# Kernel optimization log

Hardware: AMD Instinct MI355X
Metric: run time of the kernel (lower is better)

The kernel has to match this reference:

```python
import jax, jax.numpy as jnp
import numpy as np

NUM_GRAPHS = 1024


def setup_inputs() -> dict:
    key = jax.random.key(0)
    k1, k2, k3, k4 = jax.random.split(key, 4)
    N, D, H = 500000, 256, 256
    x = jax.random.normal(k1, (N, D), dtype=jnp.float32)
    batch = jnp.sort(jax.random.randint(k2, (N,), 0, NUM_GRAPHS, dtype=jnp.int64))
    # Linear init scale ~ 1/sqrt(fan_in)
    W1 = jax.random.normal(k3, (D, H), dtype=jnp.float32) / np.sqrt(D)
    b1 = jnp.zeros((H,), dtype=jnp.float32)
    W2 = jax.random.normal(k4, (H, 1), dtype=jnp.float32) / np.sqrt(H)
    b2 = jnp.zeros((1,), dtype=jnp.float32)
    return {"x": x, "batch": batch, "W1": W1, "b1": b1, "W2": W2, "b2": b2}


def reference(x, batch, W1, b1, W2, b2):
    # Two-layer attention MLP -> scores [N, 1] (dropout = identity at eval)
    scores = jnp.tanh(x @ W1 + b1) @ W2 + b2
    # Softmax over dim 0 (global over all nodes, as in the source)
    attn = jax.nn.softmax(scores, axis=0)  # [N, 1]
    # Weighted scatter-add pooling per graph id
    pooled = jax.ops.segment_sum(x * attn, batch, num_segments=NUM_GRAPHS)
    return pooled  # [NUM_GRAPHS, D]
```

## Files before the change

### kernel.cpp

```cpp
#include <hip/hip_runtime.h>
#include <stdint.h>

#define NBLOCKS 256
#define WPB 16
#define SLOTS (NBLOCKS * WPB)
#define SMEM_BYTES (131072 + 2048)

typedef __attribute__((ext_vector_type(8))) short bfrag_t;
typedef __attribute__((ext_vector_type(4))) float f32x4;

static __device__ __forceinline__ unsigned short f2bf(float f) {
  unsigned int u = __float_as_uint(f);
  u += 0x7fffu + ((u >> 16) & 1u);
  return (unsigned short)(u >> 16);
}

static __device__ __forceinline__ float tanh_fast(float s) {
  float e = __builtin_exp2f(s * 2.8853900817779268f);
  float r = __builtin_amdgcn_rcpf(1.f + e);
  return __builtin_fmaf(-2.f, r, 1.f);
}

static __device__ __forceinline__ float readlane_f(float v, int l) {
  return __uint_as_float(__builtin_amdgcn_readlane(__float_as_uint(v), l));
}

static __device__ __forceinline__ bfrag_t pack8(f32x4 a, f32x4 b) {
  union { bfrag_t v; unsigned int u[4]; } r;
  asm("v_cvt_pk_bf16_f32 %0, %1, %2" : "=v"(r.u[0]) : "v"(a[0]), "v"(a[1]));
  asm("v_cvt_pk_bf16_f32 %0, %1, %2" : "=v"(r.u[1]) : "v"(a[2]), "v"(a[3]));
  asm("v_cvt_pk_bf16_f32 %0, %1, %2" : "=v"(r.u[2]) : "v"(b[0]), "v"(b[1]));
  asm("v_cvt_pk_bf16_f32 %0, %1, %2" : "=v"(r.u[3]) : "v"(b[2]), "v"(b[3]));
  return r.v;
}

#define KEEPA(A) asm volatile("" : "+v"(A[0]), "+v"(A[1]), "+v"(A[2]), "+v"(A[3]), \
                                    "+v"(A[4]), "+v"(A[5]), "+v"(A[6]), "+v"(A[7]))

#define GLD16(gp, lp) __builtin_amdgcn_global_load_lds( \
    (const __attribute__((address_space(1))) void*)(gp), \
    (__attribute__((address_space(3))) void*)(lp), 16, 0, 0)

__global__ void prep_w1_kernel(const float* __restrict__ W1, unsigned short* __restrict__ W1f) {
  const int bx = blockIdx.x;
  const int l = threadIdx.x;
  const int cc = bx >> 3, kk = bx & 7;
  const int h = cc * 16 + (l & 15);
  const int kbase = kk * 32 + ((l >> 4) << 3);
  bfrag_t pk;
#pragma unroll
  for (int j = 0; j < 8; ++j) pk[j] = (short)f2bf(W1[(size_t)(kbase + j) * 256 + h]);
  *(bfrag_t*)(W1f + (size_t)(bx * 64 + l) * 8) = pk;
}

__launch_bounds__(1024, 4)
__global__ void attnpool_kernel(const float* __restrict__ x,
                                const int* __restrict__ batch,
                                const unsigned short* __restrict__ W1f,
                                const float* __restrict__ b1,
                                const float* __restrict__ W2,
                                const float* __restrict__ b2,
                                float* __restrict__ out,
                                float* __restrict__ Zp,
                                int N, int ntiles, int tps) {
  extern __shared__ char smem[];
  char*  Bl  = smem;
  float* b1s = (float*)(smem + 131072);
  float* w2s = (float*)(smem + 132096);

  const int t = threadIdx.x;
  const int lane = t & 63;
  const int wv = t >> 6;
  const int l15 = lane & 15;
  const int hi = lane >> 4;

#pragma unroll
  for (int i = 0; i < 8; ++i) {
    const int f = wv * 8 + i;
    const unsigned short* src = W1f + (size_t)f * 512 + lane * 8;
    GLD16(src, Bl + f * 1024);
  }
  if (t < 256) { b1s[t] = b1[t]; w2s[t] = W2[t]; }
  __syncthreads();

  const float b2c = b2[0];
  const int slot = blockIdx.x * WPB + wv;
  const int t0 = slot * tps;
  const int t1 = min(t0 + tps, ntiles);

  float zacc = 0.f;
  f32x4 pacc = {0.f, 0.f, 0.f, 0.f};
  int gcur = -1;
  const char* bwave = Bl + lane * 16;

  for (int tile = t0; tile < t1; ++tile) {
    const int R0 = tile * 32;

    int bid = 0;
    {
      int rg = min(R0 + (lane & 31), N - 1);
      bid = batch[rg];
    }

    bfrag_t A0[8], A1[8];
    {
      const int r0g = min(R0 + l15, N - 1);
      const int r1g = min(R0 + 16 + l15, N - 1);
      const float* p0 = x + (size_t)r0g * 256 + hi * 8;
      const float* p1 = x + (size_t)r1g * 256 + hi * 8;
#pragma unroll
      for (int kk = 0; kk < 8; ++kk) {
        const f32x4 u0 = *(const f32x4*)(p0 + kk * 32);
        const f32x4 u1 = *(const f32x4*)(p0 + kk * 32 + 4);
        const f32x4 v0 = *(const f32x4*)(p1 + kk * 32);
        const f32x4 v1 = *(const f32x4*)(p1 + kk * 32 + 4);
        A0[kk] = pack8(u0, u1);
        A1[kk] = pack8(v0, v1);
      }
    }

    float s0[4] = {0.f, 0.f, 0.f, 0.f};
    float s1[4] = {0.f, 0.f, 0.f, 0.f};
#pragma unroll 2
    for (int cc = 0; cc < 16; ++cc) {
      KEEPA(A0);
      KEEPA(A1);
      const char* bb = bwave + cc * 8192;
      f32x4 acc0 = {0.f, 0.f, 0.f, 0.f}, acc1 = {0.f, 0.f, 0.f, 0.f};
#pragma unroll
      for (int kk = 0; kk < 8; ++kk) {
        const bfrag_t Bk = *(const bfrag_t*)(bb + kk * 1024);
        acc0 = __builtin_amdgcn_mfma_f32_16x16x32_bf16(A0[kk], Bk, acc0, 0, 0, 0);
        acc1 = __builtin_amdgcn_mfma_f32_16x16x32_bf16(A1[kk], Bk, acc1, 0, 0, 0);
      }
      const float b1c = b1s[cc * 16 + l15];
      const float w2c = w2s[cc * 16 + l15];
#pragma unroll
      for (int r = 0; r < 4; ++r) {
        s0[r] += tanh_fast(acc0[r] + b1c) * w2c;
        s1[r] += tanh_fast(acc1[r] + b1c) * w2c;
      }
    }

    float w0[4], w1[4];
#pragma unroll
    for (int r = 0; r < 4; ++r) {
      float v0 = s0[r], v1 = s1[r];
      v0 += __shfl_xor(v0, 1); v0 += __shfl_xor(v0, 2);
      v0 += __shfl_xor(v0, 4); v0 += __shfl_xor(v0, 8);
      v1 += __shfl_xor(v1, 1); v1 += __shfl_xor(v1, 2);
      v1 += __shfl_xor(v1, 4); v1 += __shfl_xor(v1, 8);
      w0[r] = (R0 + hi * 4 + r < N) ? __expf(v0 + b2c) : 0.f;
      w1[r] = (R0 + 16 + hi * 4 + r < N) ? __expf(v1 + b2c) : 0.f;
    }
    {
      float z = w0[0] + w0[1] + w0[2] + w0[3] + w1[0] + w1[1] + w1[2] + w1[3];
      z += __shfl_xor(z, 16);
      z += __shfl_xor(z, 32);
      zacc += z;
    }

    const float* xp = x + (size_t)R0 * 256 + lane * 4;
#pragma unroll
    for (int r = 0; r < 32; ++r) {
      const float wr = (r < 16) ? readlane_f(w0[r & 3], ((r >> 2) & 3) * 16)
                                : readlane_f(w1[r & 3], ((r >> 2) & 3) * 16);
      const int g = __builtin_amdgcn_readlane(bid, r);
      if (g != gcur) {
        if (gcur >= 0) {
          float* po = out + (size_t)gcur * 256 + lane * 4;
          atomicAdd(po + 0, pacc[0]); atomicAdd(po + 1, pacc[1]);
          atomicAdd(po + 2, pacc[2]); atomicAdd(po + 3, pacc[3]);
        }
        pacc[0] = pacc[1] = pacc[2] = pacc[3] = 0.f;
        gcur = g;
      }
      const f32x4 xv = *(const f32x4*)(xp + (size_t)r * 256);
      pacc[0] = __builtin_fmaf(wr, xv[0], pacc[0]);
      pacc[1] = __builtin_fmaf(wr, xv[1], pacc[1]);
      pacc[2] = __builtin_fmaf(wr, xv[2], pacc[2]);
      pacc[3] = __builtin_fmaf(wr, xv[3], pacc[3]);
    }
  }

  if (gcur >= 0) {
    float* po = out + (size_t)gcur * 256 + lane * 4;
    atomicAdd(po + 0, pacc[0]); atomicAdd(po + 1, pacc[1]);
    atomicAdd(po + 2, pacc[2]); atomicAdd(po + 3, pacc[3]);
  }
  if (lane == 0 && zacc != 0.f) atomicAdd(Zp, zacc);
}

__global__ void finalize_kernel(float* __restrict__ out, const float* __restrict__ Zp, int n4) {
  const int i = blockIdx.x * blockDim.x + threadIdx.x;
  if (i < n4) {
    const float zi = 1.f / Zp[0];
    f32x4* p = (f32x4*)out;
    f32x4 v = p[i];
    v[0] *= zi; v[1] *= zi; v[2] *= zi; v[3] *= zi;
    p[i] = v;
  }
}

extern "C" void kernel_launch(void* const* d_in, const int* in_sizes, int n_in,
                              void* d_out, int out_size, void* d_ws, size_t ws_size,
                              hipStream_t stream) {
  const float* x  = (const float*)d_in[0];
  const int* batch = (const int*)d_in[1];
  const float* W1 = (const float*)d_in[2];
  const float* b1 = (const float*)d_in[3];
  const float* W2 = (const float*)d_in[4];
  const float* b2 = (const float*)d_in[5];
  float* out = (float*)d_out;
  const int N = in_sizes[1];

  unsigned short* W1f = (unsigned short*)d_ws;
  float* Zp = (float*)((char*)d_ws + 131072);

  static int attr_done = 0;
  if (!attr_done) {
    hipFuncSetAttribute((const void*)attnpool_kernel,
                        hipFuncAttributeMaxDynamicSharedMemorySize, SMEM_BYTES);
    attr_done = 1;
  }

  const int ntiles = (N + 31) / 32;
  const int tps = (ntiles + SLOTS - 1) / SLOTS;

  hipMemsetAsync(d_out, 0, (size_t)out_size * sizeof(float), stream);
  hipMemsetAsync(Zp, 0, sizeof(float), stream);
  prep_w1_kernel<<<128, 64, 0, stream>>>(W1, W1f);
  attnpool_kernel<<<NBLOCKS, 1024, SMEM_BYTES, stream>>>(x, batch, W1f, b1, W2, b2,
                                                         out, Zp, N, ntiles, tps);
  finalize_kernel<<<(out_size / 4 + 255) / 256, 256, 0, stream>>>(out, Zp, out_size / 4);
}
```

Baseline: 214.1 us.

## Reuse bf16 register fragments of x for pooling instead of reloading x

Pooling now accumulates from the bf16 A fragments already held in registers for the MFMA, removing the second global read of x per tile. Per-row weights are broadcast through a small LDS slot, partial sums are reduced with lane shuffles, and multi-graph tiles are handled with masked per-segment passes. This trades memory traffic for extra ALU and shuffle work, and pooling precision drops from fp32 to bf16-rounded x.

```diff
diff --git a/kernel.cpp b/kernel.cpp
--- a/kernel.cpp
+++ b/kernel.cpp
@@ -4,7 +4,7 @@
 #define NBLOCKS 256
 #define WPB 16
 #define SLOTS (NBLOCKS * WPB)
-#define SMEM_BYTES (131072 + 2048)
+#define SMEM_BYTES (131072 + 1024 + 1024 + 2048)
 
 typedef __attribute__((ext_vector_type(8))) short bfrag_t;
 typedef __attribute__((ext_vector_type(4))) float f32x4;
@@ -19,10 +19,6 @@
   float e = __builtin_exp2f(s * 2.8853900817779268f);
   float r = __builtin_amdgcn_rcpf(1.f + e);
   return __builtin_fmaf(-2.f, r, 1.f);
-}
-
-static __device__ __forceinline__ float readlane_f(float v, int l) {
-  return __uint_as_float(__builtin_amdgcn_readlane(__float_as_uint(v), l));
 }
 
 static __device__ __forceinline__ bfrag_t pack8(f32x4 a, f32x4 b) {
@@ -67,6 +63,7 @@
   char*  Bl  = smem;
   float* b1s = (float*)(smem + 131072);
   float* w2s = (float*)(smem + 132096);
+  float* wsl = (float*)(smem + 133120);
 
   const int t = threadIdx.x;
   const int lane = t & 63;
@@ -89,20 +86,82 @@
   const int t1 = min(t0 + tps, ntiles);
 
   float zacc = 0.f;
-  f32x4 pacc = {0.f, 0.f, 0.f, 0.f};
+  float pacc[16];
+#pragma unroll
+  for (int i = 0; i < 16; ++i) pacc[i] = 0.f;
   int gcur = -1;
   const char* bwave = Bl + lane * 16;
+  float* ws = wsl + (wv << 5);
+
+  bfrag_t A0[8], A1[8];
+
+  auto flush = [&]() {
+#pragma unroll
+    for (int i = 0; i < 16; ++i) {
+      pacc[i] += __shfl_xor(pacc[i], 4);
+      pacc[i] += __shfl_xor(pacc[i], 8);
+    }
+    if (l15 < 4) {
+      float* po = out + (size_t)gcur * 256 + hi * 8 + 2 * l15;
+#pragma unroll
+      for (int i = 0; i < 16; ++i)
+        atomicAdd(po + (i >> 1) * 32 + (i & 1), pacc[i]);
+    }
+#pragma unroll
+    for (int i = 0; i < 16; ++i) pacc[i] = 0.f;
+  };
+
+  auto pool_pass = [&](float m0, float m1) {
+    const bool s0 = (l15 & 1) != 0, s1 = (l15 & 2) != 0;
+#pragma unroll
+    for (int half = 0; half < 2; ++half) {
+      float part[4][4][2];
+#pragma unroll
+      for (int k2 = 0; k2 < 4; ++k2) {
+        const int kk = half * 4 + k2;
+        union { bfrag_t v; unsigned int u[4]; } ua, ub;
+        ua.v = A0[kk]; ub.v = A1[kk];
+#pragma unroll
+        for (int q = 0; q < 4; ++q) {
+          const float alo = __uint_as_float(ua.u[q] << 16);
+          const float ahi = __uint_as_float(ua.u[q] & 0xffff0000u);
+          const float blo = __uint_as_float(ub.u[q] << 16);
+          const float bhi = __uint_as_float(ub.u[q] & 0xffff0000u);
+          part[k2][q][0] = __builtin_fmaf(m0, alo, m1 * blo);
+          part[k2][q][1] = __builtin_fmaf(m0, ahi, m1 * bhi);
+        }
+      }
+#pragma unroll
+      for (int k2 = 0; k2 < 4; ++k2)
+#pragma unroll
+        for (int q = 0; q < 4; ++q)
+#pragma unroll
+          for (int p = 0; p < 2; ++p) {
+            float v = part[k2][q][p];
+            v += __shfl_xor(v, 1);
+            v += __shfl_xor(v, 2);
+            part[k2][q][p] = v;
+          }
+#pragma unroll
+      for (int k2 = 0; k2 < 4; ++k2)
+#pragma unroll
+        for (int p = 0; p < 2; ++p) {
+          const float v01 = s0 ? part[k2][1][p] : part[k2][0][p];
+          const float v23 = s0 ? part[k2][3][p] : part[k2][2][p];
+          pacc[(half * 4 + k2) * 2 + p] += s1 ? v23 : v01;
+        }
+    }
+  };
 
   for (int tile = t0; tile < t1; ++tile) {
     const int R0 = tile * 32;
 
-    int bid = 0;
+    int bid;
     {
-      int rg = min(R0 + (lane & 31), N - 1);
+      const int rg = min(R0 + (lane & 31), N - 1);
       bid = batch[rg];
     }
 
-    bfrag_t A0[8], A1[8];
     {
       const int r0g = min(R0 + l15, N - 1);
       const int r1g = min(R0 + 16 + l15, N - 1);
@@ -119,8 +178,8 @@
       }
     }
 
-    float s0[4] = {0.f, 0.f, 0.f, 0.f};
-    float s1[4] = {0.f, 0.f, 0.f, 0.f};
+    float s0v[4] = {0.f, 0.f, 0.f, 0.f};
+    float s1v[4] = {0.f, 0.f, 0.f, 0.f};
 #pragma unroll 2
     for (int cc = 0; cc < 16; ++cc) {
       KEEPA(A0);
@@ -137,57 +196,57 @@
       const float w2c = w2s[cc * 16 + l15];
 #pragma unroll
       for (int r = 0; r < 4; ++r) {
-        s0[r] += tanh_fast(acc0[r] + b1c) * w2c;
-        s1[r] += tanh_fast(acc1[r] + b1c) * w2c;
-      }
-    }
-
-    float w0[4], w1[4];
+        s0v[r] += tanh_fast(acc0[r] + b1c) * w2c;
+        s1v[r] += tanh_fast(acc1[r] + b1c) * w2c;
+      }
+    }
+
+    f32x4 w0v, w1v;
 #pragma unroll
     for (int r = 0; r < 4; ++r) {
-      float v0 = s0[r], v1 = s1[r];
+      float v0 = s0v[r], v1 = s1v[r];
       v0 += __shfl_xor(v0, 1); v0 += __shfl_xor(v0, 2);
       v0 += __shfl_xor(v0, 4); v0 += __shfl_xor(v0, 8);
       v1 += __shfl_xor(v1, 1); v1 += __shfl_xor(v1, 2);
       v1 += __shfl_xor(v1, 4); v1 += __shfl_xor(v1, 8);
-      w0[r] = (R0 + hi * 4 + r < N) ? __expf(v0 + b2c) : 0.f;
-      w1[r] = (R0 + 16 + hi * 4 + r < N) ? __expf(v1 + b2c) : 0.f;
+      w0v[r] = (R0 + hi * 4 + r < N) ? __expf(v0 + b2c) : 0.f;
+      w1v[r] = (R0 + 16 + hi * 4 + r < N) ? __expf(v1 + b2c) : 0.f;
     }
     {
-      float z = w0[0] + w0[1] + w0[2] + w0[3] + w1[0] + w1[1] + w1[2] + w1[3];
+      float z = w0v[0] + w0v[1] + w0v[2] + w0v[3] + w1v[0] + w1v[1] + w1v[2] + w1v[3];
       z += __shfl_xor(z, 16);
       z += __shfl_xor(z, 32);
       zacc += z;
     }
 
-    const float* xp = x + (size_t)R0 * 256 + lane * 4;
-#pragma unroll
-    for (int r = 0; r < 32; ++r) {
-      const float wr = (r < 16) ? readlane_f(w0[r & 3], ((r >> 2) & 3) * 16)
-                                : readlane_f(w1[r & 3], ((r >> 2) & 3) * 16);
-      const int g = __builtin_amdgcn_readlane(bid, r);
-      if (g != gcur) {
-        if (gcur >= 0) {
-          float* po = out + (size_t)gcur * 256 + lane * 4;
-          atomicAdd(po + 0, pacc[0]); atomicAdd(po + 1, pacc[1]);
-          atomicAdd(po + 2, pacc[2]); atomicAdd(po + 3, pacc[3]);
-        }
-        pacc[0] = pacc[1] = pacc[2] = pacc[3] = 0.f;
-        gcur = g;
-      }
-      const f32x4 xv = *(const f32x4*)(xp + (size_t)r * 256);
-      pacc[0] = __builtin_fmaf(wr, xv[0], pacc[0]);
-      pacc[1] = __builtin_fmaf(wr, xv[1], pacc[1]);
-      pacc[2] = __builtin_fmaf(wr, xv[2], pacc[2]);
-      pacc[3] = __builtin_fmaf(wr, xv[3], pacc[3]);
-    }
-  }
-
-  if (gcur >= 0) {
-    float* po = out + (size_t)gcur * 256 + lane * 4;
-    atomicAdd(po + 0, pacc[0]); atomicAdd(po + 1, pacc[1]);
-    atomicAdd(po + 2, pacc[2]); atomicAdd(po + 3, pacc[3]);
-  }
+    if (l15 == 0) {
+      *(f32x4*)(ws + hi * 4) = w0v;
+      *(f32x4*)(ws + 16 + hi * 4) = w1v;
+    }
+    const float w0f = ws[l15];
+    const float w1f = ws[l15 + 16];
+
+    const int g_first = __builtin_amdgcn_readlane(bid, 0);
+    const int g_last  = __builtin_amdgcn_readlane(bid, 31);
+    if (g_first == g_last) {
+      if (g_first != gcur) { if (gcur >= 0) flush(); gcur = g_first; }
+      pool_pass(w0f, w1f);
+    } else {
+      int s = 0;
+      while (s < 32) {
+        const int g = __builtin_amdgcn_readlane(bid, s);
+        int e = s + 1;
+        while (e < 32 && __builtin_amdgcn_readlane(bid, e) == g) ++e;
+        if (g != gcur) { if (gcur >= 0) flush(); gcur = g; }
+        const float m0 = (l15 >= s && l15 < e) ? w0f : 0.f;
+        const float m1 = (16 + l15 >= s && 16 + l15 < e) ? w1f : 0.f;
+        pool_pass(m0, m1);
+        s = e;
+      }
+    }
+  }
+
+  if (gcur >= 0) flush();
   if (lane == 0 && zacc != 0.f) atomicAdd(Zp, zacc);
 }
 
```

After: 323.7 us. +51.2%, slower.
